# Optimization experiments

Measured on AMD Instinct MI355X. Metric: run time of the kernel, lower is better.

Reference implementation:

```python
import jax, jax.numpy as jnp
import numpy as np

N_HEAD = 16
N_KV = 4
Q_PER_KV = N_HEAD // N_KV  # 4
HEAD_DIM = 64
SCALE = HEAD_DIM ** -0.5


def setup_inputs() -> dict:
    key = jax.random.key(0)
    k1, k2, k3, k4 = jax.random.split(key, 4)
    B, L, H = 2, 2048, 1024
    x = jax.random.normal(k1, (B, L, H), dtype=jnp.float32)
    Wq = jax.random.normal(k2, (H, H), dtype=jnp.float32) * 0.02
    Wkv = jax.random.normal(k3, (2 * H // Q_PER_KV, H), dtype=jnp.float32) * 0.02
    Wo = jax.random.normal(k4, (H, H), dtype=jnp.float32) * 0.02
    return {"x": x, "Wq": Wq, "Wkv": Wkv, "Wo": Wo}


def reference(x, Wq, Wkv, Wo):
    B, L, H = x.shape
    # projections (nn.Linear: y = x @ W.T)
    q = (x @ Wq.T).reshape(B, L, N_KV, Q_PER_KV, HEAD_DIM)
    kv = (x @ Wkv.T).reshape(B, L, N_KV, 2, HEAD_DIM)
    k = kv[:, :, :, 0, :]  # [B, L, N_KV, D]
    v = kv[:, :, :, 1, :]  # [B, L, N_KV, D]
    # scores: [B, n_kv, q_per_kv, L, L]
    qk = SCALE * jnp.einsum('blgpd,bmgd->bgplm', q, k)
    qk = qk.reshape(B, N_HEAD, L, L)
    # ALiBi: slope_h * tril(j - i)
    slopes = 2.0 ** (-8.0 / N_HEAD * (jnp.arange(N_HEAD, dtype=jnp.float32) + 1.0))
    pos = jnp.arange(L)
    rel = jnp.tril(pos[None, :] - pos[:, None]).astype(qk.dtype)  # [L, L]
    qk = qk + slopes[:, None, None] * rel[None]
    # causal mask
    causal = pos[None, :] <= pos[:, None]  # [L, L] lower-triangular True
    qk = jnp.where(causal[None, None], qk, -jnp.inf)
    score = jax.nn.softmax(qk, axis=-1).reshape(B, N_KV, Q_PER_KV, L, L)
    # attend values: [B, n_kv, q_per_kv, L, D]
    out = jnp.einsum('bgplm,bmgd->bgpld', score, v)
    out = out.reshape(B, N_HEAD, L, HEAD_DIM).transpose(0, 2, 1, 3).reshape(B, L, H)
    return out @ Wo.T
```

## Files before the change

kernel.cpp:

```cpp
#include <hip/hip_runtime.h>

typedef unsigned short u16;
typedef unsigned int u32;
typedef float f32x4 __attribute__((ext_vector_type(4)));
typedef float f32x16 __attribute__((ext_vector_type(16)));
typedef __bf16 bf16x8 __attribute__((ext_vector_type(8)));
typedef u32 u32x4 __attribute__((ext_vector_type(4)));

__device__ __forceinline__ u16 f2bf(float f) {
  u32 u = __builtin_bit_cast(u32, f);
  u32 r = (u + 0x7fffu + ((u >> 16) & 1u)) >> 16;
  return (u16)r;
}

__device__ __forceinline__ u32 pk2bf(float lo, float hi_) {
  u32 r;
  asm("v_cvt_pk_bf16_f32 %0, %1, %2" : "=v"(r) : "v"(lo), "v"(hi_));
  return r;
}

__device__ __forceinline__ void plswap(u32 &a, u32 &b) {
#if __has_builtin(__builtin_amdgcn_permlane32_swap)
  auto r = __builtin_amdgcn_permlane32_swap(a, b, false, false);
  a = r[0]; b = r[1];
#else
  asm volatile("v_permlane32_swap_b32 %0, %1" : "+v"(a), "+v"(b));
#endif
}

__device__ __forceinline__ float xhalf_max(float x) {
  u32 a = __builtin_bit_cast(u32, x), b = a;
  plswap(a, b);
  return fmaxf(__builtin_bit_cast(float, a), __builtin_bit_cast(float, b));
}
__device__ __forceinline__ float xhalf_sum(float x) {
  u32 a = __builtin_bit_cast(u32, x), b = a;
  plswap(a, b);
  return __builtin_bit_cast(float, a) + __builtin_bit_cast(float, b);
}

__global__ __launch_bounds__(256) void cvt_kernel(
    const float4* __restrict__ x, const float4* __restrict__ wq,
    const float4* __restrict__ wkv, const float4* __restrict__ wo,
    uint2* __restrict__ xb, uint2* __restrict__ wqkvb, uint2* __restrict__ wob) {
  long i = (long)blockIdx.x * 256 + threadIdx.x;
  const float4* src; uint2* dst; long off;
  if (i < 1048576)      { src = x;   dst = xb;             off = i; }
  else if (i < 1310720) { src = wq;  dst = wqkvb;          off = i - 1048576; }
  else if (i < 1441792) { src = wkv; dst = wqkvb + 262144; off = i - 1310720; }
  else                  { src = wo;  dst = wob;            off = i - 1441792; }
  float4 v = src[off];
  uint2 o;
  o.x = ((u32)f2bf(v.y) << 16) | (u32)f2bf(v.x);
  o.y = ((u32)f2bf(v.w) << 16) | (u32)f2bf(v.z);
  dst[off] = o;
}

__device__ __forceinline__ void gemm_core(
    const u16* __restrict__ A, const u16* __restrict__ W, int K,
    f32x4 acc[4][4], u16 As[128][40], u16 Ws[128][40]) {
  const int t = threadIdx.x;
  const int lane = t & 63;
  const int w = t >> 6;
  const int wm = (w >> 1) * 64, wn = (w & 1) * 64;
  const long bm = (long)blockIdx.x * 128, bn = (long)blockIdx.y * 128;
  const int sr = t >> 2;
  const int sc = (t & 3) * 8;
  const int cc = lane & 15;
  const int kg8 = (lane >> 4) * 8;

#pragma unroll
  for (int i = 0; i < 4; i++)
#pragma unroll
    for (int j = 0; j < 4; j++) acc[i][j] = f32x4{0.f, 0.f, 0.f, 0.f};

  for (int k0 = 0; k0 < K; k0 += 32) {
    *(uint4*)&As[sr][sc]      = *(const uint4*)&A[(bm + sr) * K + k0 + sc];
    *(uint4*)&As[sr + 64][sc] = *(const uint4*)&A[(bm + sr + 64) * K + k0 + sc];
    *(uint4*)&Ws[sr][sc]      = *(const uint4*)&W[(bn + sr) * K + k0 + sc];
    *(uint4*)&Ws[sr + 64][sc] = *(const uint4*)&W[(bn + sr + 64) * K + k0 + sc];
    __syncthreads();
    bf16x8 af[4], wf[4];
#pragma unroll
    for (int i = 0; i < 4; i++) af[i] = *(const bf16x8*)&As[wm + i * 16 + cc][kg8];
#pragma unroll
    for (int j = 0; j < 4; j++) wf[j] = *(const bf16x8*)&Ws[wn + j * 16 + cc][kg8];
#pragma unroll
    for (int i = 0; i < 4; i++)
#pragma unroll
      for (int j = 0; j < 4; j++)
        acc[i][j] = __builtin_amdgcn_mfma_f32_16x16x32_bf16(af[i], wf[j], acc[i][j], 0, 0, 0);
    __syncthreads();
  }
}

__global__ __launch_bounds__(256) void gemm_qkv_kernel(
    const u16* __restrict__ A, const u16* __restrict__ W,
    u16* __restrict__ Qb, u16* __restrict__ Kb, u16* __restrict__ VTb) {
  __shared__ __align__(16) u16 As[128][40];
  __shared__ __align__(16) u16 Ws[128][40];
  f32x4 acc[4][4];
  gemm_core(A, W, 1024, acc, As, Ws);
  const int t = threadIdx.x, lane = t & 63, w = t >> 6;
  const int wm = (w >> 1) * 64, wn = (w & 1) * 64;
  const int bm = blockIdx.x * 128, bn = blockIdx.y * 128;
  const int rr = (lane >> 4) * 4, cc = lane & 15;
#pragma unroll
  for (int i = 0; i < 4; i++)
#pragma unroll
    for (int jf = 0; jf < 4; jf++)
#pragma unroll
      for (int j = 0; j < 4; j++) {
        int m = bm + wm + i * 16 + rr + j;
        int n = bn + wn + jf * 16 + cc;
        float v = acc[i][jf][j];
        if (n < 1024) {
          Qb[(long)m * 1024 + n] = f2bf(v * 0.18033688011112043f);
        } else {
          int c = n - 1024, g = c >> 7, rm = c & 127;
          int b = m >> 11, pos = m & 2047;
          long base = (long)(b * 4 + g);
          if (rm < 64) Kb[(base * 2048 + pos) * 64 + rm] = f2bf(v);
          else         VTb[(base * 64 + (rm - 64)) * 2048 + pos] = f2bf(v);
        }
      }
}

__global__ __launch_bounds__(256) void gemm_out_kernel(
    const u16* __restrict__ A, const u16* __restrict__ W, float* __restrict__ out) {
  __shared__ __align__(16) u16 As[128][40];
  __shared__ __align__(16) u16 Ws[128][40];
  f32x4 acc[4][4];
  gemm_core(A, W, 1024, acc, As, Ws);
  const int t = threadIdx.x, lane = t & 63, w = t >> 6;
  const int wm = (w >> 1) * 64, wn = (w & 1) * 64;
  const int bm = blockIdx.x * 128, bn = blockIdx.y * 128;
  const int rr = (lane >> 4) * 4, cc = lane & 15;
#pragma unroll
  for (int i = 0; i < 4; i++)
#pragma unroll
    for (int jf = 0; jf < 4; jf++)
#pragma unroll
      for (int j = 0; j < 4; j++) {
        int m = bm + wm + i * 16 + rr + j;
        int n = bn + wn + jf * 16 + cc;
        out[(long)m * 1024 + n] = acc[i][jf][j];
      }
}

__global__ __launch_bounds__(256, 4) void attn_kernel(
    const u16* __restrict__ Q, const u16* __restrict__ Kb,
    const u16* __restrict__ VTb, u16* __restrict__ AT) {
  __shared__ __align__(16) float Ol[4][32][68];
  __shared__ float ml[4][2][32];

  const int t = threadIdx.x, lane = t & 63, w = t >> 6;
  const int qt = 63 - (int)blockIdx.x;
  const int h = blockIdx.y, b = blockIdx.z;
  const int g = h >> 2;
  const int lam = lane & 31, hi = lane >> 5;
  const int qrow0 = qt * 32;
  const int kblocks = (qrow0 + 95) >> 6;

  const u16* Qrow = Q + ((long)(b * 2048 + qrow0 + lam)) * 1024 + h * 64 + hi * 8;
  bf16x8 qf0 = *(const bf16x8*)(Qrow);
  bf16x8 qf1 = *(const bf16x8*)(Qrow + 16);
  bf16x8 qf2 = *(const bf16x8*)(Qrow + 32);
  bf16x8 qf3 = *(const bf16x8*)(Qrow + 48);

  const u16* Kg = Kb  + ((long)(b * 4 + g)) * 2048 * 64;
  const u16* Vg = VTb + ((long)(b * 4 + g)) * 64 * 2048;

  f32x16 zv;
#pragma unroll
  for (int i = 0; i < 16; i++) zv[i] = 0.f;
  f32x16 acc0 = zv, acc1 = zv;
  float m = -1e30f, lsum = 0.f;

  const float slope2 = exp2f(-0.5f * (float)(h + 1)) * 1.44269504f;
  const float fqr = (float)(qrow0 + lam);

  auto qk_tile = [&](int koff) -> f32x16 {
    const u16* Ka = Kg + (long)(koff + lam) * 64 + hi * 8;
    bf16x8 k0 = *(const bf16x8*)(Ka);
    bf16x8 k1 = *(const bf16x8*)(Ka + 16);
    bf16x8 k2 = *(const bf16x8*)(Ka + 32);
    bf16x8 k3 = *(const bf16x8*)(Ka + 48);
    f32x16 s = zv;
    s = __builtin_amdgcn_mfma_f32_32x32x16_bf16(k0, qf0, s, 0, 0, 0);
    s = __builtin_amdgcn_mfma_f32_32x32x16_bf16(k1, qf1, s, 0, 0, 0);
    s = __builtin_amdgcn_mfma_f32_32x32x16_bf16(k2, qf2, s, 0, 0, 0);
    s = __builtin_amdgcn_mfma_f32_32x32x16_bf16(k3, qf3, s, 0, 0, 0);
    float kb0 = (float)(koff + 4 * hi) - fqr;
    if (koff + 31 > qrow0) {
#pragma unroll
      for (int r = 0; r < 16; r++) {
        float d = kb0 + (float)((r & 3) + 8 * (r >> 2));
        s[r] = (d > 0.f) ? -1e30f : s[r] + slope2 * d;
      }
    } else {
#pragma unroll
      for (int r = 0; r < 16; r++)
        s[r] += slope2 * (kb0 + (float)((r & 3) + 8 * (r >> 2)));
    }
    return s;
  };

  auto pv_tile = [&](const f32x16 &p, int koff) {
    u32 wd[8];
#pragma unroll
    for (int i = 0; i < 8; i++) wd[i] = pk2bf(p[2 * i], p[2 * i + 1]);
    plswap(wd[0], wd[2]); plswap(wd[1], wd[3]);
    plswap(wd[4], wd[6]); plswap(wd[5], wd[7]);
    bf16x8 pf0 = __builtin_bit_cast(bf16x8, u32x4{wd[0], wd[1], wd[2], wd[3]});
    bf16x8 pf1 = __builtin_bit_cast(bf16x8, u32x4{wd[4], wd[5], wd[6], wd[7]});
    const u16* Va = Vg + (long)lam * 2048 + koff + hi * 8;
    bf16x8 v00 = *(const bf16x8*)(Va);
    bf16x8 v01 = *(const bf16x8*)(Va + 16);
    bf16x8 v10 = *(const bf16x8*)(Va + 32 * 2048);
    bf16x8 v11 = *(const bf16x8*)(Va + 32 * 2048 + 16);
    acc0 = __builtin_amdgcn_mfma_f32_32x32x16_bf16(v00, pf0, acc0, 0, 0, 0);
    acc0 = __builtin_amdgcn_mfma_f32_32x32x16_bf16(v01, pf1, acc0, 0, 0, 0);
    acc1 = __builtin_amdgcn_mfma_f32_32x32x16_bf16(v10, pf0, acc1, 0, 0, 0);
    acc1 = __builtin_amdgcn_mfma_f32_32x32x16_bf16(v11, pf1, acc1, 0, 0, 0);
  };

  for (int jb = w; jb < kblocks; jb += 4) {
    const int kbase = jb * 64;
    f32x16 st0 = qk_tile(kbase);
    f32x16 st1;
    const bool t1v = (kbase + 32 <= qrow0 + 31);
    if (t1v) {
      st1 = qk_tile(kbase + 32);
    } else {
#pragma unroll
      for (int r = 0; r < 16; r++) st1[r] = -1e30f;
    }

    float red[8];
#pragma unroll
    for (int i = 0; i < 8; i++)
      red[i] = fmaxf(fmaxf(st0[i], st0[i + 8]), fmaxf(st1[i], st1[i + 8]));
#pragma unroll
    for (int i = 0; i < 4; i++) red[i] = fmaxf(red[i], red[i + 4]);
    float pm = fmaxf(fmaxf(red[0], red[1]), fmaxf(red[2], red[3]));
    pm = xhalf_max(pm);
    float mnew = fmaxf(m, pm);
    float al = exp2f(m - mnew);
    m = mnew;
    lsum *= al;
    acc0 *= al;
    acc1 *= al;
#pragma unroll
    for (int r = 0; r < 16; r++) st0[r] = exp2f(st0[r] - m);
#pragma unroll
    for (int r = 0; r < 16; r++) st1[r] = exp2f(st1[r] - m);
    {
      float sr[8];
#pragma unroll
      for (int i = 0; i < 8; i++) sr[i] = (st0[i] + st0[i + 8]) + (st1[i] + st1[i + 8]);
#pragma unroll
      for (int i = 0; i < 4; i++) sr[i] += sr[i + 4];
      float rs = (sr[0] + sr[1]) + (sr[2] + sr[3]);
      lsum += xhalf_sum(rs);
    }

    pv_tile(st0, kbase);
    if (t1v) pv_tile(st1, kbase + 32);
  }

#pragma unroll
  for (int rq = 0; rq < 4; rq++) {
    *(f32x4*)&Ol[w][lam][8 * rq + 4 * hi] =
        f32x4{acc0[4 * rq], acc0[4 * rq + 1], acc0[4 * rq + 2], acc0[4 * rq + 3]};
    *(f32x4*)&Ol[w][lam][32 + 8 * rq + 4 * hi] =
        f32x4{acc1[4 * rq], acc1[4 * rq + 1], acc1[4 * rq + 2], acc1[4 * rq + 3]};
  }
  if (hi == 0) { ml[w][0][lam] = m; ml[w][1][lam] = lsum; }
  __syncthreads();

  const int r = t >> 3, c0 = (t & 7) * 8;
  float M = fmaxf(fmaxf(ml[0][0][r], ml[1][0][r]), fmaxf(ml[2][0][r], ml[3][0][r]));
  float o[8];
#pragma unroll
  for (int i = 0; i < 8; i++) o[i] = 0.f;
  float L = 0.f;
#pragma unroll
  for (int ww = 0; ww < 4; ww++) {
    float sc = exp2f(ml[ww][0][r] - M);
    L += sc * ml[ww][1][r];
#pragma unroll
    for (int i = 0; i < 8; i++) o[i] += sc * Ol[ww][r][c0 + i];
  }
  float inv = 1.f / L;
  uint4 ov;
  ov.x = ((u32)f2bf(o[1] * inv) << 16) | f2bf(o[0] * inv);
  ov.y = ((u32)f2bf(o[3] * inv) << 16) | f2bf(o[2] * inv);
  ov.z = ((u32)f2bf(o[5] * inv) << 16) | f2bf(o[4] * inv);
  ov.w = ((u32)f2bf(o[7] * inv) << 16) | f2bf(o[6] * inv);
  *(uint4*)&AT[((long)(b * 2048 + qrow0 + r)) * 1024 + h * 64 + c0] = ov;
}

extern "C" void kernel_launch(void* const* d_in, const int* in_sizes, int n_in,
                              void* d_out, int out_size, void* d_ws, size_t ws_size,
                              hipStream_t stream) {
  const float* x   = (const float*)d_in[0];
  const float* Wq  = (const float*)d_in[1];
  const float* Wkv = (const float*)d_in[2];
  const float* Wo  = (const float*)d_in[3];
  float* out = (float*)d_out;
  char* ws = (char*)d_ws;

  u16* xb    = (u16*)(ws);
  u16* wqkvb = (u16*)(ws + 8388608);
  u16* wob   = (u16*)(ws + 11534336);
  u16* Qb    = (u16*)(ws + 13631488);
  u16* Kb    = (u16*)(ws + 22020096);
  u16* VTb   = (u16*)(ws + 24117248);
  u16* AT    = (u16*)(ws + 26214400);

  cvt_kernel<<<6656, 256, 0, stream>>>(
      (const float4*)x, (const float4*)Wq, (const float4*)Wkv, (const float4*)Wo,
      (uint2*)xb, (uint2*)wqkvb, (uint2*)wob);

  gemm_qkv_kernel<<<dim3(32, 12), 256, 0, stream>>>(xb, wqkvb, Qb, Kb, VTb);

  attn_kernel<<<dim3(64, 16, 2), 256, 0, stream>>>(Qb, Kb, VTb, AT);

  gemm_out_kernel<<<dim3(32, 8), 256, 0, stream>>>(AT, wob, out);
}
```

Before: 237.1 us.

## Use direct global-to-LDS loads in GEMMs and slim attention LDS for occupancy

The GEMM core now loads A/W tiles with global_load_lds into unpadded 32-wide LDS tiles, skipping the register round-trip. The attention kernel halves its output-merge LDS buffer by merging the two 32-column halves in two passes, and raises launch bounds to 8 blocks per CU. It also iterates key blocks in reverse and skips the online-softmax rescale when the new max exceeds the old by no more than 8 (a lazy-rescale threshold). Unpadded LDS rows may cause bank conflicts on fragment reads, and the extra barriers add sync cost.

```diff
diff --git a/kernel.cpp b/kernel.cpp
--- a/kernel.cpp
+++ b/kernel.cpp
@@ -37,6 +37,12 @@
   u32 a = __builtin_bit_cast(u32, x), b = a;
   plswap(a, b);
   return __builtin_bit_cast(float, a) + __builtin_bit_cast(float, b);
+}
+
+__device__ __forceinline__ void gll16(const u16* g, u16* l) {
+  __builtin_amdgcn_global_load_lds(
+      (const __attribute__((address_space(1))) void*)g,
+      (__attribute__((address_space(3))) void*)l, 16, 0, 0);
 }
 
 __global__ __launch_bounds__(256) void cvt_kernel(
@@ -57,17 +63,23 @@
 }
 
 __device__ __forceinline__ void gemm_core(
-    const u16* __restrict__ A, const u16* __restrict__ W, int K,
-    f32x4 acc[4][4], u16 As[128][40], u16 Ws[128][40]) {
-  const int t = threadIdx.x;
-  const int lane = t & 63;
-  const int w = t >> 6;
+    const u16* __restrict__ A, const u16* __restrict__ W, const int K,
+    f32x4 acc[4][4], u16* As, u16* Ws) {
+  const int t = threadIdx.x, lane = t & 63, w = t >> 6;
   const int wm = (w >> 1) * 64, wn = (w & 1) * 64;
   const long bm = (long)blockIdx.x * 128, bn = (long)blockIdx.y * 128;
-  const int sr = t >> 2;
-  const int sc = (t & 3) * 8;
-  const int cc = lane & 15;
-  const int kg8 = (lane >> 4) * 8;
+  const int cc = lane & 15, kg8 = (lane >> 4) * 8;
+
+  const int srow = w * 32 + (lane >> 2);
+  const int scol = (lane & 3) * 8;
+  const u16* Ag0 = &A[(bm + srow) * (long)K + scol];
+  const u16* Ag1 = Ag0 + 16 * (long)K;
+  const u16* Wg0 = &W[(bn + srow) * (long)K + scol];
+  const u16* Wg1 = Wg0 + 16 * (long)K;
+  u16* Al0 = As + (w * 32) * 32;
+  u16* Al1 = Al0 + 16 * 32;
+  u16* Wl0 = Ws + (w * 32) * 32;
+  u16* Wl1 = Wl0 + 16 * 32;
 
 #pragma unroll
   for (int i = 0; i < 4; i++)
@@ -75,16 +87,16 @@
     for (int j = 0; j < 4; j++) acc[i][j] = f32x4{0.f, 0.f, 0.f, 0.f};
 
   for (int k0 = 0; k0 < K; k0 += 32) {
-    *(uint4*)&As[sr][sc]      = *(const uint4*)&A[(bm + sr) * K + k0 + sc];
-    *(uint4*)&As[sr + 64][sc] = *(const uint4*)&A[(bm + sr + 64) * K + k0 + sc];
-    *(uint4*)&Ws[sr][sc]      = *(const uint4*)&W[(bn + sr) * K + k0 + sc];
-    *(uint4*)&Ws[sr + 64][sc] = *(const uint4*)&W[(bn + sr + 64) * K + k0 + sc];
+    gll16(Ag0 + k0, Al0);
+    gll16(Ag1 + k0, Al1);
+    gll16(Wg0 + k0, Wl0);
+    gll16(Wg1 + k0, Wl1);
     __syncthreads();
     bf16x8 af[4], wf[4];
 #pragma unroll
-    for (int i = 0; i < 4; i++) af[i] = *(const bf16x8*)&As[wm + i * 16 + cc][kg8];
-#pragma unroll
-    for (int j = 0; j < 4; j++) wf[j] = *(const bf16x8*)&Ws[wn + j * 16 + cc][kg8];
+    for (int i = 0; i < 4; i++) af[i] = *(const bf16x8*)&As[(wm + i * 16 + cc) * 32 + kg8];
+#pragma unroll
+    for (int j = 0; j < 4; j++) wf[j] = *(const bf16x8*)&Ws[(wn + j * 16 + cc) * 32 + kg8];
 #pragma unroll
     for (int i = 0; i < 4; i++)
 #pragma unroll
@@ -97,8 +109,8 @@
 __global__ __launch_bounds__(256) void gemm_qkv_kernel(
     const u16* __restrict__ A, const u16* __restrict__ W,
     u16* __restrict__ Qb, u16* __restrict__ Kb, u16* __restrict__ VTb) {
-  __shared__ __align__(16) u16 As[128][40];
-  __shared__ __align__(16) u16 Ws[128][40];
+  __shared__ __align__(16) u16 As[128 * 32];
+  __shared__ __align__(16) u16 Ws[128 * 32];
   f32x4 acc[4][4];
   gemm_core(A, W, 1024, acc, As, Ws);
   const int t = threadIdx.x, lane = t & 63, w = t >> 6;
@@ -128,8 +140,8 @@
 
 __global__ __launch_bounds__(256) void gemm_out_kernel(
     const u16* __restrict__ A, const u16* __restrict__ W, float* __restrict__ out) {
-  __shared__ __align__(16) u16 As[128][40];
-  __shared__ __align__(16) u16 Ws[128][40];
+  __shared__ __align__(16) u16 As[128 * 32];
+  __shared__ __align__(16) u16 Ws[128 * 32];
   f32x4 acc[4][4];
   gemm_core(A, W, 1024, acc, As, Ws);
   const int t = threadIdx.x, lane = t & 63, w = t >> 6;
@@ -148,10 +160,10 @@
       }
 }
 
-__global__ __launch_bounds__(256, 4) void attn_kernel(
+__global__ __launch_bounds__(256, 8) void attn_kernel(
     const u16* __restrict__ Q, const u16* __restrict__ Kb,
     const u16* __restrict__ VTb, u16* __restrict__ AT) {
-  __shared__ __align__(16) float Ol[4][32][68];
+  __shared__ __align__(16) float Ol[4][32][36];
   __shared__ float ml[4][2][32];
 
   const int t = threadIdx.x, lane = t & 63, w = t >> 6;
@@ -225,7 +237,8 @@
     acc1 = __builtin_amdgcn_mfma_f32_32x32x16_bf16(v11, pf1, acc1, 0, 0, 0);
   };
 
-  for (int jb = w; jb < kblocks; jb += 4) {
+  const int jb0 = (kblocks > w) ? (w + (((kblocks - 1 - w) >> 2) << 2)) : -1;
+  for (int jb = jb0; jb >= 0; jb -= 4) {
     const int kbase = jb * 64;
     f32x16 st0 = qk_tile(kbase);
     f32x16 st1;
@@ -245,12 +258,14 @@
     for (int i = 0; i < 4; i++) red[i] = fmaxf(red[i], red[i + 4]);
     float pm = fmaxf(fmaxf(red[0], red[1]), fmaxf(red[2], red[3]));
     pm = xhalf_max(pm);
-    float mnew = fmaxf(m, pm);
-    float al = exp2f(m - mnew);
-    m = mnew;
-    lsum *= al;
-    acc0 *= al;
-    acc1 *= al;
+    if (!__all(pm <= m + 8.f)) {
+      float mnew = fmaxf(m, pm);
+      float al = exp2f(m - mnew);
+      m = mnew;
+      lsum *= al;
+      acc0 *= al;
+      acc1 *= al;
+    }
 #pragma unroll
     for (int r = 0; r < 16; r++) st0[r] = exp2f(st0[r] - m);
 #pragma unroll
@@ -270,35 +285,50 @@
   }
 
 #pragma unroll
-  for (int rq = 0; rq < 4; rq++) {
+  for (int rq = 0; rq < 4; rq++)
     *(f32x4*)&Ol[w][lam][8 * rq + 4 * hi] =
         f32x4{acc0[4 * rq], acc0[4 * rq + 1], acc0[4 * rq + 2], acc0[4 * rq + 3]};
-    *(f32x4*)&Ol[w][lam][32 + 8 * rq + 4 * hi] =
-        f32x4{acc1[4 * rq], acc1[4 * rq + 1], acc1[4 * rq + 2], acc1[4 * rq + 3]};
-  }
   if (hi == 0) { ml[w][0][lam] = m; ml[w][1][lam] = lsum; }
   __syncthreads();
 
-  const int r = t >> 3, c0 = (t & 7) * 8;
+  const int r = t >> 3, c0 = (t & 7) * 4;
   float M = fmaxf(fmaxf(ml[0][0][r], ml[1][0][r]), fmaxf(ml[2][0][r], ml[3][0][r]));
-  float o[8];
-#pragma unroll
-  for (int i = 0; i < 8; i++) o[i] = 0.f;
+  float sc[4];
   float L = 0.f;
 #pragma unroll
   for (int ww = 0; ww < 4; ww++) {
-    float sc = exp2f(ml[ww][0][r] - M);
-    L += sc * ml[ww][1][r];
-#pragma unroll
-    for (int i = 0; i < 8; i++) o[i] += sc * Ol[ww][r][c0 + i];
-  }
-  float inv = 1.f / L;
-  uint4 ov;
-  ov.x = ((u32)f2bf(o[1] * inv) << 16) | f2bf(o[0] * inv);
-  ov.y = ((u32)f2bf(o[3] * inv) << 16) | f2bf(o[2] * inv);
-  ov.z = ((u32)f2bf(o[5] * inv) << 16) | f2bf(o[4] * inv);
-  ov.w = ((u32)f2bf(o[7] * inv) << 16) | f2bf(o[6] * inv);
-  *(uint4*)&AT[((long)(b * 2048 + qrow0 + r)) * 1024 + h * 64 + c0] = ov;
+    sc[ww] = exp2f(ml[ww][0][r] - M);
+    L += sc[ww] * ml[ww][1][r];
+  }
+  const float inv = 1.f / L;
+  {
+    float o[4] = {0.f, 0.f, 0.f, 0.f};
+#pragma unroll
+    for (int ww = 0; ww < 4; ww++)
+#pragma unroll
+      for (int i = 0; i < 4; i++) o[i] += sc[ww] * Ol[ww][r][c0 + i];
+    uint2 ov;
+    ov.x = ((u32)f2bf(o[1] * inv) << 16) | f2bf(o[0] * inv);
+    ov.y = ((u32)f2bf(o[3] * inv) << 16) | f2bf(o[2] * inv);
+    *(uint2*)&AT[((long)(b * 2048 + qrow0 + r)) * 1024 + h * 64 + c0] = ov;
+  }
+  __syncthreads();
+#pragma unroll
+  for (int rq = 0; rq < 4; rq++)
+    *(f32x4*)&Ol[w][lam][8 * rq + 4 * hi] =
+        f32x4{acc1[4 * rq], acc1[4 * rq + 1], acc1[4 * rq + 2], acc1[4 * rq + 3]};
+  __syncthreads();
+  {
+    float o[4] = {0.f, 0.f, 0.f, 0.f};
+#pragma unroll
+    for (int ww = 0; ww < 4; ww++)
+#pragma unroll
+      for (int i = 0; i < 4; i++) o[i] += sc[ww] * Ol[ww][r][c0 + i];
+    uint2 ov;
+    ov.x = ((u32)f2bf(o[1] * inv) << 16) | f2bf(o[0] * inv);
+    ov.y = ((u32)f2bf(o[3] * inv) << 16) | f2bf(o[2] * inv);
+    *(uint2*)&AT[((long)(b * 2048 + qrow0 + r)) * 1024 + h * 64 + 32 + c0] = ov;
+  }
 }
 
 extern "C" void kernel_launch(void* const* d_in, const int* in_sizes, int n_in,
```

After: 849.1 us. 3.58x slower.
